# Kernel optimization log

Measured on AMD Instinct MI355X. Metric: run time of the kernel, lower is better.

Reference implementation:

```python
import jax, jax.numpy as jnp
import numpy as np

E = 1024        # embed_dim
NH = 16         # num_heads
HD = E // NH    # head_dim = 64
MLP = 4096
HID = int(2 * MLP / 3)  # 2730, TransNeXt ConvGLU hidden
NT = 1          # no_rope task tokens (skip rotary / skip dwconv)
B, S = 8, 1025
GRID = 32       # sqrt(S - NT)
EPS = 1e-6
SCALE = HD ** -0.5


def rmsnorm(x, g):
    return x * jax.lax.rsqrt(jnp.mean(x * x, axis=-1, keepdims=True) + EPS) * g


def apply_rope(t):
    # t: [B, NH, s, HD] -- rotate-half RoPE over image-token positions
    s = t.shape[2]
    pos = jnp.arange(s, dtype=jnp.float32)
    inv_freq = 1.0 / (10000.0 ** (jnp.arange(0, HD, 2, dtype=jnp.float32) / HD))
    freqs = pos[:, None] * inv_freq[None, :]          # [s, HD/2]
    cos = jnp.concatenate([jnp.cos(freqs)] * 2, -1)   # [s, HD]
    sin = jnp.concatenate([jnp.sin(freqs)] * 2, -1)
    t1, t2 = jnp.split(t, 2, axis=-1)
    rot = jnp.concatenate([-t2, t1], axis=-1)
    return t * cos + rot * sin


def rope_skip_task(t):
    # first NT tokens are task tokens -> identity; rest get rotary with positions 0..
    return jnp.concatenate([t[:, :, :NT], apply_rope(t[:, :, NT:])], axis=2)


def setup_inputs() -> dict:
    key = jax.random.key(0)
    ks = jax.random.split(key, 12)
    init = lambda k, shape, fan: (jax.random.normal(k, shape, jnp.float32) * (fan ** -0.5))
    return {
        "x": jax.random.normal(ks[0], (B, S, E), jnp.float32),
        "g1": jnp.ones((E,), jnp.float32),
        "w_qkv": init(ks[1], (E, 3 * E), E),
        "b_qkv": jnp.zeros((3 * E,), jnp.float32),
        "w_proj": init(ks[2], (E, E), E),
        "b_proj": jnp.zeros((E,), jnp.float32),
        "g2": jnp.ones((E,), jnp.float32),
        "fc1_w": init(ks[3], (E, 2 * HID), E),
        "fc1_b": jnp.zeros((2 * HID,), jnp.float32),
        "dw_w": init(ks[4], (3, 3, 1, HID), 9),  # HWIO depthwise 3x3
        "dw_b": jnp.zeros((HID,), jnp.float32),
        "fc2_w": init(ks[5], (HID, E), HID),
        "fc2_b": jnp.zeros((E,), jnp.float32),
    }


def reference(x, g1, w_qkv, b_qkv, w_proj, b_proj, g2, fc1_w, fc1_b, dw_w, dw_b, fc2_w, fc2_b):
    # ---- attention block ----
    residual = x
    xn = rmsnorm(x, g1)
    qkv = xn @ w_qkv + b_qkv                              # [B,S,3E]
    qkv = qkv.reshape(B, S, 3, NH, HD).transpose(2, 0, 3, 1, 4)
    q, k, v = qkv[0], qkv[1], qkv[2]                      # [B,NH,S,HD]
    q = rope_skip_task(q)
    k = rope_skip_task(k)
    attn = jnp.einsum("bhqd,bhkd->bhqk", q * SCALE, k)    # [B,NH,S,S]
    attn = jax.nn.softmax(attn, axis=-1)
    out = jnp.einsum("bhqk,bhkd->bhqd", attn, v)          # [B,NH,S,HD]
    out = out.transpose(0, 2, 1, 3).reshape(B, S, E)
    out = out @ w_proj + b_proj
    x = residual + out

    # ---- ConvGLU MLP block ----
    residual = x
    xn = rmsnorm(x, g2)
    h = xn @ fc1_w + fc1_b                                # [B,S,2*HID]
    xg, vg = jnp.split(h, 2, axis=-1)
    x_task, x_img = xg[:, :NT], xg[:, NT:]                # dwconv only on image tokens
    img = x_img.reshape(B, GRID, GRID, HID)
    img = jax.lax.conv_general_dilated(
        img, dw_w, window_strides=(1, 1), padding="SAME",
        feature_group_count=HID,
        dimension_numbers=("NHWC", "HWIO", "NHWC")) + dw_b
    x_img = img.reshape(B, GRID * GRID, HID)
    xc = jnp.concatenate([x_task, x_img], axis=1)
    h = jax.nn.gelu(xc, approximate=False) * vg           # GLU gate
    h = h @ fc2_w + fc2_b
    return residual + h
```

## Files before the change

kernel.cpp:

```cpp
#include <hip/hip_runtime.h>
#include <hip/hip_bf16.h>
#include <math.h>

#define E_DIM 1024
#define NHEAD 16
#define HID_DIM 2730
#define KP_FC2 2752
#define HB_LD 5504
#define XG_OFF 2752
#define FC1_N 5482
#define B_DIM 8
#define S_DIM 1025
#define EPS_V 1e-6f
#define SCALE_V 0.125f
#define MROWS (B_DIM * S_DIM)

typedef __attribute__((ext_vector_type(8))) short short8;
typedef __attribute__((ext_vector_type(4))) float f32x4;
typedef unsigned short us;

__device__ __forceinline__ float b2f(us u) {
    union { unsigned int i; float f; } x; x.i = ((unsigned int)u) << 16; return x.f;
}
__device__ __forceinline__ us f2b(float f) {
    __hip_bfloat16 h = __float2bfloat16(f);
    return *reinterpret_cast<us*>(&h);
}

__device__ __forceinline__ void stage16(const void* g, void* l) {
    __builtin_amdgcn_global_load_lds(
        (const __attribute__((address_space(1))) unsigned int*)g,
        (__attribute__((address_space(3))) unsigned int*)l,
        16, 0, 0);
}

__device__ __forceinline__ int sl(int row, int c8) {
    return (row * 8 + (c8 ^ (row & 7))) * 8;
}

#define MFMA16(a, b, c) __builtin_amdgcn_mfma_f32_16x16x32_bf16(a, b, c, 0, 0, 0)

__global__ __launch_bounds__(256) void rmsnorm_kernel(const float* __restrict__ x,
        const float* __restrict__ g, us* __restrict__ out) {
    int row = blockIdx.x;
    const float4* xr = (const float4*)(x + (size_t)row * E_DIM);
    float4 v = xr[threadIdx.x];
    float ss = v.x*v.x + v.y*v.y + v.z*v.z + v.w*v.w;
    #pragma unroll
    for (int off = 32; off > 0; off >>= 1) ss += __shfl_down(ss, off, 64);
    __shared__ float wsum[4];
    int lane = threadIdx.x & 63, w = threadIdx.x >> 6;
    if (lane == 0) wsum[w] = ss;
    __syncthreads();
    float tot = wsum[0] + wsum[1] + wsum[2] + wsum[3];
    float inv = rsqrtf(tot * (1.0f / E_DIM) + EPS_V);
    float4 gv = ((const float4*)g)[threadIdx.x];
    ushort4 o;
    o.x = f2b(v.x * inv * gv.x); o.y = f2b(v.y * inv * gv.y);
    o.z = f2b(v.z * inv * gv.z); o.w = f2b(v.w * inv * gv.w);
    ((ushort4*)(out + (size_t)row * E_DIM))[threadIdx.x] = o;
}

__global__ __launch_bounds__(256) void rmsnorm_add_kernel(float* __restrict__ x,
        const float* __restrict__ p, const float* __restrict__ g, us* __restrict__ out) {
    int row = blockIdx.x;
    float4* xr = (float4*)(x + (size_t)row * E_DIM);
    const float4* pr = (const float4*)(p + (size_t)row * E_DIM);
    float4 v = xr[threadIdx.x];
    float4 pv = pr[threadIdx.x];
    v.x += pv.x; v.y += pv.y; v.z += pv.z; v.w += pv.w;
    xr[threadIdx.x] = v;
    float ss = v.x*v.x + v.y*v.y + v.z*v.z + v.w*v.w;
    #pragma unroll
    for (int off = 32; off > 0; off >>= 1) ss += __shfl_down(ss, off, 64);
    __shared__ float wsum[4];
    int lane = threadIdx.x & 63, w = threadIdx.x >> 6;
    if (lane == 0) wsum[w] = ss;
    __syncthreads();
    float tot = wsum[0] + wsum[1] + wsum[2] + wsum[3];
    float inv = rsqrtf(tot * (1.0f / E_DIM) + EPS_V);
    float4 gv = ((const float4*)g)[threadIdx.x];
    ushort4 o;
    o.x = f2b(v.x * inv * gv.x); o.y = f2b(v.y * inv * gv.y);
    o.z = f2b(v.z * inv * gv.z); o.w = f2b(v.w * inv * gv.w);
    ((ushort4*)(out + (size_t)row * E_DIM))[threadIdx.x] = o;
}

__global__ __launch_bounds__(256) void addreduce_kernel(float* __restrict__ dst,
        const float* __restrict__ p, int n4) {
    int stride = gridDim.x * 256;
    for (int i = blockIdx.x * 256 + threadIdx.x; i < n4; i += stride) {
        float4 a = ((const float4*)p)[i];
        float4 d = ((float4*)dst)[i];
        d.x += a.x; d.y += a.y; d.z += a.z; d.w += a.w;
        ((float4*)dst)[i] = d;
    }
}

__global__ __launch_bounds__(256) void convt_kernel(const float* __restrict__ W,
        us* __restrict__ WT, int K, int N, int KPad, int swap_half, int xg_off, int Wld) {
    __shared__ float T[32][33];
    int n0 = blockIdx.x * 32, k0 = blockIdx.y * 32;
    int c = threadIdx.x & 31, r4 = (threadIdx.x >> 5) << 2;
    #pragma unroll
    for (int i = 0; i < 4; i++) {
        int k = k0 + r4 + i, n = n0 + c;
        float v = 0.0f;
        if (k < K && n < N) {
            int src = n;
            int ok = 1;
            if (swap_half) {
                if (n < swap_half) src = n + swap_half;
                else if (xg_off) { if (n >= xg_off) src = n - xg_off; else ok = 0; }
                else src = n - swap_half;
            }
            if (ok) v = W[(size_t)k * Wld + src];
        }
        T[c][r4 + i] = v;
    }
    __syncthreads();
    #pragma unroll
    for (int i = 0; i < 4; i++) {
        int n = n0 + r4 + i, k = k0 + c;
        if (n < N && k < KPad) WT[(size_t)n * KPad + k] = f2b(T[r4 + i][c]);
    }
}

__global__ __launch_bounds__(256) void bias_perm_kernel(const float* __restrict__ b,
        float* __restrict__ bp) {
    int r = blockIdx.x * 256 + threadIdx.x;
    if (r < FC1_N)
        bp[r] = (r < HID_DIM) ? b[r + HID_DIM] : ((r < XG_OFF) ? 0.0f : b[r - XG_OFF]);
}

template<int MODE>
__global__ __launch_bounds__(512, 2) void gemm256(const us* __restrict__ A, int lda,
        const us* __restrict__ Bt, int ldb, const float* __restrict__ bias,
        const float* __restrict__ Rres, void* __restrict__ Cv,
        int M, int N, int K, int ldc, int Ksplit, float* __restrict__ Pbuf) {
    __shared__ __align__(16) us lds[2][4][8192];
    us* const L = &lds[0][0][0];
    const int tid = threadIdx.x;
    const int lane = tid & 63;
    const int w = tid >> 6;
    const int wm = w >> 2, wn = w & 3;
    const int l15 = lane & 15, quad = lane >> 4;

    const int nwg = gridDim.x * gridDim.y;
    const int orig = blockIdx.y * gridDim.x + blockIdx.x;
    const int q8 = nwg >> 3, r8 = nwg & 7;
    const int xcd = orig & 7, oi = orig >> 3;
    const int wgid = (xcd < r8 ? xcd * (q8 + 1) : r8 * (q8 + 1) + (xcd - r8) * q8) + oi;
    const int m0 = (wgid / gridDim.x) * 256, n0 = (wgid % gridDim.x) * 256;

    const int kz = (MODE == 2) ? (int)blockIdx.z : 0;
    const int kofs = kz * Ksplit;
    const int Keff = (MODE == 2) ? (kz ? K - Ksplit : Ksplit) : K;

    const int r0 = tid >> 3;
    const int c80 = (tid & 7) ^ (r0 & 7);
    const us* const pA = A + (size_t)(m0 + r0) * lda + kofs + c80 * 8;
    const us* const pB = Bt + (size_t)(n0 + r0) * ldb + kofs + c80 * 8;
    const size_t a64 = (size_t)64 * lda, b64 = (size_t)64 * ldb;
    us* const dst = L + tid * 8;

#define STG_A(b, h, kt) do { \
    const us* s_ = pA + (size_t)(h) * 2 * a64 + (size_t)(kt) * 64; \
    stage16(s_,       dst + ((b) * 4 + (h)) * 8192); \
    stage16(s_ + a64, dst + ((b) * 4 + (h)) * 8192 + 4096); \
} while (0)
#define STG_B(b, h, kt) do { \
    const us* s_ = pB + (size_t)(h) * 2 * b64 + (size_t)(kt) * 64; \
    stage16(s_,       dst + ((b) * 4 + 2 + (h)) * 8192); \
    stage16(s_ + b64, dst + ((b) * 4 + 2 + (h)) * 8192 + 4096); \
} while (0)

    f32x4 acc[8][4];
    #pragma unroll
    for (int m = 0; m < 8; m++)
        #pragma unroll
        for (int n = 0; n < 4; n++) acc[m][n] = (f32x4){0.f, 0.f, 0.f, 0.f};

    const int nk = Keff >> 6;
    const int brow = (wn & 1) * 64;

    STG_A(0, 0, 0); STG_A(0, 1, 0);
    STG_B(0, 0, 0); STG_B(0, 1, 0);
    if (nk > 1) {
        STG_B(1, 0, 1); STG_B(1, 1, 1);
        STG_A(1, 0, 1); STG_A(1, 1, 1);
        asm volatile("s_waitcnt vmcnt(8)" ::: "memory");
    } else {
        asm volatile("s_waitcnt vmcnt(0)" ::: "memory");
    }
    __builtin_amdgcn_s_barrier();
    __builtin_amdgcn_sched_barrier(0);

    short8 bf01[2][2];
    {
        const us* bB0 = L + (2 + (wn >> 1)) * 8192;
        #pragma unroll
        for (int n = 0; n < 2; n++) {
            bf01[n][0] = *(const short8*)(bB0 + sl(brow + n * 16 + l15, quad));
            bf01[n][1] = *(const short8*)(bB0 + sl(brow + n * 16 + l15, 4 + quad));
        }
    }

    for (int t = 0; t < nk; t++) {
        const int c = t & 1, cn = c ^ 1;
        const us* aB = L + (c * 4 + wm) * 8192;
        const us* bB = L + (c * 4 + 2 + (wn >> 1)) * 8192;
        const us* bBn = L + (cn * 4 + 2 + (wn >> 1)) * 8192;
        short8 bf2[2][2];
        #pragma unroll
        for (int n = 0; n < 2; n++) {
            bf2[n][0] = *(const short8*)(bB + sl(brow + (n + 2) * 16 + l15, quad));
            bf2[n][1] = *(const short8*)(bB + sl(brow + (n + 2) * 16 + l15, 4 + quad));
        }
        #pragma unroll
        for (int p = 0; p < 4; p++) {
            const int mp = 2 * p;
            short8 a00 = *(const short8*)(aB + sl(mp * 16 + l15, quad));
            short8 a01 = *(const short8*)(aB + sl(mp * 16 + l15, 4 + quad));
            short8 a10 = *(const short8*)(aB + sl(mp * 16 + 16 + l15, quad));
            short8 a11 = *(const short8*)(aB + sl(mp * 16 + 16 + l15, 4 + quad));
            if (p == 1) { if (t + 2 < nk) STG_B(c, 0, t + 2); }
            else if (p == 2) { if (t + 2 < nk) STG_B(c, 1, t + 2); }
            else if (p == 3) {
                if (t + 2 < nk)      { asm volatile("s_waitcnt vmcnt(4)" ::: "memory"); }
                else if (t + 1 < nk) { asm volatile("s_waitcnt vmcnt(0)" ::: "memory"); }
            }
            __builtin_amdgcn_s_barrier();
            if (p == 3) __builtin_amdgcn_sched_barrier(0);
            __builtin_amdgcn_s_setprio(1);
            #pragma unroll
            for (int n = 0; n < 4; n++) {
                const short8 b0 = (n < 2) ? bf01[n][0] : bf2[n - 2][0];
                const short8 b1 = (n < 2) ? bf01[n][1] : bf2[n - 2][1];
                acc[mp][n]     = MFMA16(a00, b0, acc[mp][n]);
                acc[mp][n]     = MFMA16(a01, b1, acc[mp][n]);
                acc[mp + 1][n] = MFMA16(a10, b0, acc[mp + 1][n]);
                acc[mp + 1][n] = MFMA16(a11, b1, acc[mp + 1][n]);
            }
            __builtin_amdgcn_s_setprio(0);
            if (p == 3) {
                if (t + 2 < nk) { STG_A(c, 0, t + 2); STG_A(c, 1, t + 2); }
                if (t + 1 < nk) {
                    #pragma unroll
                    for (int n = 0; n < 2; n++) {
                        bf01[n][0] = *(const short8*)(bBn + sl(brow + n * 16 + l15, quad));
                        bf01[n][1] = *(const short8*)(bBn + sl(brow + n * 16 + l15, 4 + quad));
                    }
                }
            }
            __builtin_amdgcn_s_barrier();
            if (p == 3) __builtin_amdgcn_sched_barrier(0);
        }
    }

    #pragma unroll
    for (int m = 0; m < 8; m++) {
        int gm0 = m0 + wm * 128 + m * 16 + quad * 4;
        #pragma unroll
        for (int n = 0; n < 4; n++) {
            int gn = n0 + wn * 64 + n * 16 + l15;
            if (gn >= N) continue;
            float bs = (MODE == 2) ? (kz == 0 ? bias[gn] : 0.0f) : bias[gn];
            #pragma unroll
            for (int r = 0; r < 4; r++) {
                int gm = gm0 + r;
                if (gm >= M) continue;
                float v = acc[m][n][r] + bs;
                if (MODE == 0) {
                    ((us*)Cv)[(size_t)gm * ldc + gn] = f2b(v);
                } else if (MODE == 1) {
                    ((float*)Cv)[(size_t)gm * ldc + gn] = v + Rres[(size_t)gm * ldc + gn];
                } else {
                    if (kz == 0)
                        ((float*)Cv)[(size_t)gm * ldc + gn] = v + Rres[(size_t)gm * ldc + gn];
                    else
                        Pbuf[(size_t)gm * ldc + gn] = v;
                }
            }
        }
    }
#undef STG_A
#undef STG_B
}

__global__ __launch_bounds__(256) void rope_kernel(us* __restrict__ qkv) {
    int idx = blockIdx.x * 256 + threadIdx.x;
    int i = idx & 31;
    int h = (idx >> 5) & (NHEAD - 1);
    int rc = idx >> 9;
    int s = rc % S_DIM;
    us* q = qkv + (size_t)rc * 3072 + h * 64;
    us* k = q + 1024;
    if (s == 0) {
        q[i] = f2b(b2f(q[i]) * SCALE_V);
        q[i + 32] = f2b(b2f(q[i + 32]) * SCALE_V);
        return;
    }
    float pos = (float)(s - 1);
    float invf = expf((float)i * (-9.210340371976184f / 32.0f));
    float f = pos * invf;
    float c = cosf(f), sn = sinf(f);
    float q1 = b2f(q[i]), q2 = b2f(q[i + 32]);
    q[i]      = f2b((q1 * c - q2 * sn) * SCALE_V);
    q[i + 32] = f2b((q2 * c + q1 * sn) * SCALE_V);
    float k1 = b2f(k[i]), k2 = b2f(k[i + 32]);
    k[i]      = f2b(k1 * c - k2 * sn);
    k[i + 32] = f2b(k2 * c + k1 * sn);
}

__global__ __launch_bounds__(256) void vtrans_kernel(const us* __restrict__ qkv,
        us* __restrict__ Vt) {
    __shared__ us T[64][65];
    int st = blockIdx.x, h = blockIdx.y, bc = blockIdx.z;
    int tid = threadIdx.x;
    int r = tid & 63, cb = (tid >> 6) * 16;
    const us* src = qkv + (size_t)(bc * S_DIM + st * 64 + r) * 3072 + 2048 + h * 64 + cb;
    #pragma unroll
    for (int i = 0; i < 4; i++) {
        ushort4 v = *(const ushort4*)(src + i * 4);
        T[cb + i*4 + 0][r] = v.x; T[cb + i*4 + 1][r] = v.y;
        T[cb + i*4 + 2][r] = v.z; T[cb + i*4 + 3][r] = v.w;
    }
    __syncthreads();
    int d = tid >> 2, sc = (tid & 3) * 16;
    us* dstp = Vt + ((size_t)((bc * 16 + h) * 64 + d)) * 1088 + st * 64 + sc;
    #pragma unroll
    for (int g = 0; g < 4; g++) {
        ushort4 o;
        int i0 = sc + g * 4;
        o.x = (st*64 + i0 + 0 < S_DIM) ? T[d][i0 + 0] : 0;
        o.y = (st*64 + i0 + 1 < S_DIM) ? T[d][i0 + 1] : 0;
        o.z = (st*64 + i0 + 2 < S_DIM) ? T[d][i0 + 2] : 0;
        o.w = (st*64 + i0 + 3 < S_DIM) ? T[d][i0 + 3] : 0;
        *(ushort4*)(dstp + g * 4) = o;
    }
}

__global__ __launch_bounds__(256) void attn_kernel(const us* __restrict__ qkv,
        const us* __restrict__ Vt, us* __restrict__ attnb) {
    __shared__ __align__(16) us Kb[2][4096];
    __shared__ __align__(16) us Vb[2][4096];
    __shared__ __align__(16) us Ps[4096];
    int qt = blockIdx.x, h = blockIdx.y, bc = blockIdx.z;
    int tid = threadIdx.x;
    int lane = tid & 63, w = tid >> 6;
    int l15 = lane & 15, quad = lane >> 4;

    const us* qrow = qkv + (size_t)(bc * S_DIM + qt * 64 + 16 * w + l15) * 3072 + h * 64;
    short8 qa0 = *(const short8*)(qrow + quad * 8);
    short8 qa1 = *(const short8*)(qrow + 32 + quad * 8);

    const us* kg = qkv + (size_t)(bc * S_DIM) * 3072 + 1024 + h * 64;
    const us* vgp = Vt + (size_t)((bc * 16 + h) * 64) * 1088;

    int s0 = tid, s1 = 256 + tid;
    int row0 = s0 >> 3, c8_0 = (s0 & 7) ^ (row0 & 7);
    int row1 = s1 >> 3, c8_1 = (s1 & 7) ^ (row1 & 7);

    f32x4 acc_o[4];
    float mr[4], lr[4];
    #pragma unroll
    for (int r = 0; r < 4; r++) { mr[r] = -1e30f; lr[r] = 0.f; }
    #pragma unroll
    for (int j = 0; j < 4; j++) acc_o[j] = (f32x4){0.f, 0.f, 0.f, 0.f};

    stage16(kg + (size_t)row0 * 3072 + c8_0 * 8, Kb[0] + s0 * 8);
    stage16(vgp + (size_t)row0 * 1088 + c8_0 * 8, Vb[0] + s0 * 8);
    stage16(kg + (size_t)row1 * 3072 + c8_1 * 8, Kb[0] + s1 * 8);
    stage16(vgp + (size_t)row1 * 1088 + c8_1 * 8, Vb[0] + s1 * 8);
    __syncthreads();

    for (int kt = 0; kt < 17; kt++) {
        int cur = kt & 1, nxt = cur ^ 1;
        if (kt + 1 < 17) {
            stage16(kg + (size_t)((kt + 1) * 64 + row0) * 3072 + c8_0 * 8, Kb[nxt] + s0 * 8);
            stage16(vgp + (size_t)row0 * 1088 + (kt + 1) * 64 + c8_0 * 8, Vb[nxt] + s0 * 8);
            stage16(kg + (size_t)((kt + 1) * 64 + row1) * 3072 + c8_1 * 8, Kb[nxt] + s1 * 8);
            stage16(vgp + (size_t)row1 * 1088 + (kt + 1) * 64 + c8_1 * 8, Vb[nxt] + s1 * 8);
        }

        f32x4 accS[4];
        #pragma unroll
        for (int j = 0; j < 4; j++) accS[j] = (f32x4){0.f, 0.f, 0.f, 0.f};
        __builtin_amdgcn_s_setprio(1);
        #pragma unroll
        for (int j = 0; j < 4; j++) {
            short8 kb0 = *(const short8*)(Kb[cur] + sl(16 * j + l15, quad));
            short8 kb1 = *(const short8*)(Kb[cur] + sl(16 * j + l15, 4 + quad));
            accS[j] = MFMA16(qa0, kb0, accS[j]);
            accS[j] = MFMA16(qa1, kb1, accS[j]);
        }
        __builtin_amdgcn_s_setprio(0);

        #pragma unroll
        for (int j = 0; j < 4; j++) {
            if (kt * 64 + 16 * j + l15 >= S_DIM) {
                #pragma unroll
                for (int r = 0; r < 4; r++) accS[j][r] = -1e30f;
            }
        }

        float tm[4];
        #pragma unroll
        for (int r = 0; r < 4; r++) {
            float t = fmaxf(fmaxf(accS[0][r], accS[1][r]), fmaxf(accS[2][r], accS[3][r]));
            #pragma unroll
            for (int off = 1; off < 16; off <<= 1)
                t = fmaxf(t, __shfl_xor(t, off, 64));
            tm[r] = t;
        }
        int need = (tm[0] > mr[0] + 8.f) || (tm[1] > mr[1] + 8.f) ||
                   (tm[2] > mr[2] + 8.f) || (tm[3] > mr[3] + 8.f);
        if (__any(need)) {
            #pragma unroll
            for (int r = 0; r < 4; r++) {
                float mnew = fmaxf(mr[r], tm[r]);
                float al = __expf(mr[r] - mnew);
                mr[r] = mnew;
                lr[r] *= al;
                #pragma unroll
                for (int j = 0; j < 4; j++) acc_o[j][r] *= al;
            }
        }
        float pr[4][4];
        #pragma unroll
        for (int r = 0; r < 4; r++) {
            float rs = 0.f;
            #pragma unroll
            for (int j = 0; j < 4; j++) {
                float p = __expf(accS[j][r] - mr[r]);
                pr[j][r] = p;
                rs += p;
            }
            lr[r] += rs;
        }
        #pragma unroll
        for (int j = 0; j < 4; j++) {
            #pragma unroll
            for (int r = 0; r < 4; r++) {
                int prow = quad * 4 + r;
                int idx = sl(16 * w + prow, 2 * j + (l15 >> 3)) + (l15 & 7);
                Ps[idx] = f2b(pr[j][r]);
            }
        }
        short8 pa0 = *(const short8*)(Ps + sl(16 * w + l15, quad));
        short8 pa1 = *(const short8*)(Ps + sl(16 * w + l15, 4 + quad));
        __builtin_amdgcn_s_setprio(1);
        #pragma unroll
        for (int j = 0; j < 4; j++) {
            short8 vb0 = *(const short8*)(Vb[cur] + sl(16 * j + l15, quad));
            short8 vb1 = *(const short8*)(Vb[cur] + sl(16 * j + l15, 4 + quad));
            acc_o[j] = MFMA16(pa0, vb0, acc_o[j]);
            acc_o[j] = MFMA16(pa1, vb1, acc_o[j]);
        }
        __builtin_amdgcn_s_setprio(0);
        __syncthreads();
    }

    #pragma unroll
    for (int r = 0; r < 4; r++) {
        #pragma unroll
        for (int off = 1; off < 16; off <<= 1)
            lr[r] += __shfl_xor(lr[r], off, 64);
    }
    #pragma unroll
    for (int r = 0; r < 4; r++) {
        int s = qt * 64 + 16 * w + quad * 4 + r;
        if (s >= S_DIM) continue;
        float invl = 1.0f / lr[r];
        #pragma unroll
        for (int j = 0; j < 4; j++)
            attnb[(size_t)(bc * S_DIM + s) * E_DIM + h * 64 + 16 * j + l15] =
                f2b(acc_o[j][r] * invl);
    }
}

__global__ __launch_bounds__(256) void conv_gelu_kernel(us* __restrict__ hb,
        const float* __restrict__ dw_w, const float* __restrict__ dw_b) {
    int p = blockIdx.x % S_DIM;
    size_t row = blockIdx.x;
    size_t brow = row - p;
    int pp = p - 1;
    int gy = pp >> 5, gx = pp & 31;
    for (int g = threadIdx.x; g < 342; g += 256) {
        int c0 = g * 8;
        if (c0 + 8 <= HID_DIM) {
            float val[8];
            if (p == 0) {
                short8 xv = *(const short8*)(hb + row * HB_LD + XG_OFF + c0);
                #pragma unroll
                for (int e = 0; e < 8; e++) val[e] = b2f((us)xv[e]);
            } else {
                #pragma unroll
                for (int e = 0; e < 8; e++) val[e] = dw_b[c0 + e];
                #pragma unroll
                for (int dy = 0; dy < 3; dy++) {
                    int ny = gy + dy - 1;
                    if (ny < 0 || ny >= 32) continue;
                    #pragma unroll
                    for (int dx = 0; dx < 3; dx++) {
                        int nx = gx + dx - 1;
                        if (nx < 0 || nx >= 32) continue;
                        short8 xv = *(const short8*)(hb +
                                (brow + 1 + ny * 32 + nx) * HB_LD + XG_OFF + c0);
                        const float* wp = dw_w + (dy * 3 + dx) * HID_DIM + c0;
                        float2 w0 = *(const float2*)(wp);
                        float2 w1 = *(const float2*)(wp + 2);
                        float2 w2 = *(const float2*)(wp + 4);
                        float2 w3 = *(const float2*)(wp + 6);
                        val[0] = fmaf(b2f((us)xv[0]), w0.x, val[0]);
                        val[1] = fmaf(b2f((us)xv[1]), w0.y, val[1]);
                        val[2] = fmaf(b2f((us)xv[2]), w1.x, val[2]);
                        val[3] = fmaf(b2f((us)xv[3]), w1.y, val[3]);
                        val[4] = fmaf(b2f((us)xv[4]), w2.x, val[4]);
                        val[5] = fmaf(b2f((us)xv[5]), w2.y, val[5]);
                        val[6] = fmaf(b2f((us)xv[6]), w3.x, val[6]);
                        val[7] = fmaf(b2f((us)xv[7]), w3.y, val[7]);
                    }
                }
            }
            short8 gv = *(const short8*)(hb + row * HB_LD + c0);
            short8 o;
            #pragma unroll
            for (int e = 0; e < 8; e++) {
                float ge = 0.5f * val[e] * (1.0f + erff(val[e] * 0.70710678118654752f));
                o[e] = (short)f2b(ge * b2f((us)gv[e]));
            }
            *(short8*)(hb + row * HB_LD + c0) = o;
        } else {
            for (int c = c0; c < HID_DIM; c++) {
                float val;
                if (p == 0) {
                    val = b2f(hb[row * HB_LD + XG_OFF + c]);
                } else {
                    float a = dw_b[c];
                    #pragma unroll
                    for (int dy = 0; dy < 3; dy++) {
                        int ny = gy + dy - 1;
                        if (ny < 0 || ny >= 32) continue;
                        #pragma unroll
                        for (int dx = 0; dx < 3; dx++) {
                            int nx = gx + dx - 1;
                            if (nx < 0 || nx >= 32) continue;
                            a = fmaf(b2f(hb[(brow + 1 + ny * 32 + nx) * HB_LD + XG_OFF + c]),
                                     dw_w[(dy * 3 + dx) * HID_DIM + c], a);
                        }
                    }
                    val = a;
                }
                float ge = 0.5f * val * (1.0f + erff(val * 0.70710678118654752f));
                hb[row * HB_LD + c] = f2b(ge * b2f(hb[row * HB_LD + c]));
            }
        }
    }
}

static size_t ws_need(int cb) {
    size_t R = (size_t)cb * 1025, Rp = ((R + 127) / 128) * 128;
    size_t end1 = Rp*1024*2 + Rp*3072*2 + (size_t)cb*16*64*1088*2
                + 8320ull*1024*2 + 3072ull*1024*2 + 1024ull*1024*2;
    size_t end2 = Rp*1024*2 + Rp*HB_LD*2 + 5504ull*1024*2 + 1024ull*KP_FC2*2 + 5504*4;
    return end1 > end2 ? end1 : end2;
}

extern "C" void kernel_launch(void* const* d_in, const int* in_sizes, int n_in,
                              void* d_out, int out_size, void* d_ws, size_t ws_size,
                              hipStream_t stream) {
    const float* x      = (const float*)d_in[0];
    const float* g1     = (const float*)d_in[1];
    const float* w_qkv  = (const float*)d_in[2];
    const float* b_qkv  = (const float*)d_in[3];
    const float* w_proj = (const float*)d_in[4];
    const float* b_proj = (const float*)d_in[5];
    const float* g2     = (const float*)d_in[6];
    const float* fc1_w  = (const float*)d_in[7];
    const float* fc1_b  = (const float*)d_in[8];
    const float* dw_w   = (const float*)d_in[9];
    const float* dw_b   = (const float*)d_in[10];
    const float* fc2_w  = (const float*)d_in[11];
    const float* fc2_b  = (const float*)d_in[12];
    float* out = (float*)d_out;
    char* base = (char*)d_ws;

    int CB = 2;
    if (ws_size >= ws_need(8)) CB = 8;
    else if (ws_size >= ws_need(4)) CB = 4;
    int NC = B_DIM / CB;
    size_t R = (size_t)CB * 1025, Rp = ((R + 127) / 128) * 128;
    int gy256 = (int)((R + 255) / 256);
    int gyM = (MROWS + 255) / 256;

    size_t pOff = ((ws_need(CB) + 255) / 256) * 256;
    size_t pBytes = (size_t)MROWS * E_DIM * 4;
    int use_split = (ws_size >= pOff + pBytes);
    float* P1 = (float*)(base + pOff);

    us* xn    = (us*)base;
    size_t o  = Rp * 1024 * 2;
    us* qkv   = (us*)(base + o);
    us* hbuf  = (us*)(base + o);
    size_t o2 = o + Rp * 3072 * 2;
    us* Vt    = (us*)(base + o2);
    size_t o3 = o2 + (size_t)CB * 16 * 64 * 1088 * 2;
    us* attnb = (us*)(base + o3);
    size_t o4 = o3 + 8320ull * 1024 * 2;
    us* qkvT  = (us*)(base + o4);
    size_t o5 = o4 + 3072ull * 1024 * 2;
    us* projT = (us*)(base + o5);
    size_t p2 = o + Rp * HB_LD * 2;
    us* fc1T  = (us*)(base + p2);
    size_t p3 = p2 + 5504ull * 1024 * 2;
    us* fc2T  = (us*)(base + p3);
    float* fc1bp = (float*)(base + p3 + 1024ull * KP_FC2 * 2);

    convt_kernel<<<dim3(96, 32), 256, 0, stream>>>(w_qkv, qkvT, 1024, 3072, 1024, 0, 0, 3072);
    convt_kernel<<<dim3(32, 32), 256, 0, stream>>>(w_proj, projT, 1024, 1024, 1024, 0, 0, 1024);
    for (int c = 0; c < NC; c++) {
        size_t roff = (size_t)c * R;
        rmsnorm_kernel<<<(int)R, 256, 0, stream>>>(x + roff * E_DIM, g1, xn);
        gemm256<0><<<dim3(12, gy256), 512, 0, stream>>>(xn, 1024, qkvT, 1024,
                b_qkv, nullptr, qkv, (int)R, 3072, 1024, 3072, 0, nullptr);
        rope_kernel<<<(int)(2 * R), 256, 0, stream>>>(qkv);
        vtrans_kernel<<<dim3(17, 16, CB), 256, 0, stream>>>(qkv, Vt);
        attn_kernel<<<dim3(17, 16, CB), 256, 0, stream>>>(qkv, Vt, attnb + roff * E_DIM);
    }
    if (use_split) {
        gemm256<2><<<dim3(4, gyM, 2), 512, 0, stream>>>(attnb, 1024, projT, 1024,
                b_proj, x, out, MROWS, 1024, 1024, 1024, 512, P1);
    } else {
        gemm256<1><<<dim3(4, gyM), 512, 0, stream>>>(attnb, 1024, projT, 1024,
                b_proj, x, out, MROWS, 1024, 1024, 1024, 0, nullptr);
    }

    convt_kernel<<<dim3(172, 32), 256, 0, stream>>>(fc1_w, fc1T, 1024, FC1_N, 1024,
            HID_DIM, XG_OFF, 5460);
    convt_kernel<<<dim3(32, 86), 256, 0, stream>>>(fc2_w, fc2T, HID_DIM, 1024, KP_FC2,
            0, 0, 1024);
    bias_perm_kernel<<<22, 256, 0, stream>>>(fc1_b, fc1bp);
    for (int c = 0; c < NC; c++) {
        size_t roff = (size_t)c * R;
        float* outc = out + roff * E_DIM;
        if (use_split) {
            rmsnorm_add_kernel<<<(int)R, 256, 0, stream>>>(outc, P1 + roff * E_DIM, g2, xn);
        } else {
            rmsnorm_kernel<<<(int)R, 256, 0, stream>>>(outc, g2, xn);
        }
        gemm256<0><<<dim3(22, gy256), 512, 0, stream>>>(xn, 1024, fc1T, 1024,
                fc1bp, nullptr, hbuf, (int)R, FC1_N, 1024, HB_LD, 0, nullptr);
        conv_gelu_kernel<<<(int)R, 256, 0, stream>>>(hbuf, dw_w, dw_b);
        if (use_split) {
            gemm256<2><<<dim3(4, gy256, 2), 512, 0, stream>>>(hbuf, HB_LD, fc2T, KP_FC2,
                    fc2_b, outc, outc, (int)R, 1024, KP_FC2, 1024, 1408, P1 + roff * E_DIM);
            addreduce_kernel<<<2048, 256, 0, stream>>>(outc, P1 + roff * E_DIM,
                    (int)(R * 256));
        } else {
            gemm256<1><<<dim3(4, gy256), 512, 0, stream>>>(hbuf, HB_LD, fc2T, KP_FC2,
                    fc2_b, outc, outc, (int)R, 1024, KP_FC2, 1024, 0, nullptr);
        }
    }
}
```

Baseline: 783.1 us.

## Add software-pipelined GEMM variant with XCD-aware tile remap for fc1

Adds a new 256x256 bf16 MFMA GEMM kernel used only for the fc1 projection. It double-buffers LDS stages two K-tiles ahead, interleaves global loads with MFMA phases under explicit waitcnt, barriers and priority hints, and remaps workgroup IDs so neighbouring tiles land on the same XCD for L2 reuse. The aim is to hide global-load latency and improve cache locality in the largest GEMM. The price is a large, hand-scheduled kernel whose behaviour depends on compiler scheduling and occupancy (launch bounds of 2 blocks with 128KB LDS).

```diff
diff --git a/kernel.cpp b/kernel.cpp
--- a/kernel.cpp
+++ b/kernel.cpp
@@ -286,6 +286,127 @@
     }
 #undef STG_A
 #undef STG_B
+}
+
+__global__ __launch_bounds__(512, 2) void gemm256v2(const us* __restrict__ A, int lda,
+        const us* __restrict__ Bt, int ldb, const float* __restrict__ bias,
+        void* __restrict__ Cv, int M, int N, int K, int ldc) {
+    __shared__ __align__(16) us lds[2][32768];
+    us* const L = &lds[0][0];
+    const int tid = threadIdx.x;
+    const int lane = tid & 63;
+    const int w = tid >> 6;
+    const int wm = w >> 2, wn = w & 3;
+    const int l15 = lane & 15, quad = lane >> 4;
+
+    const int nwg = gridDim.x * gridDim.y;
+    const int orig = blockIdx.y * gridDim.x + blockIdx.x;
+    const int q8 = nwg >> 3, r8 = nwg & 7;
+    const int xcd = orig & 7, oi = orig >> 3;
+    const int wgid = (xcd < r8 ? xcd * (q8 + 1) : r8 * (q8 + 1) + (xcd - r8) * q8) + oi;
+    const int m0 = (wgid / gridDim.x) * 256, n0 = (wgid % gridDim.x) * 256;
+
+    const int a_lr = (tid >> 3) & 31;
+    const int a_c8 = (tid & 7) ^ (a_lr & 7);
+    const us* const pA2 = A + (size_t)(m0 + ((tid >> 8) << 7) + a_lr) * lda + a_c8 * 8;
+    const int r0 = tid >> 3;
+    const int c80 = (tid & 7) ^ (r0 & 7);
+    const us* const pB = Bt + (size_t)(n0 + r0) * ldb + c80 * 8;
+    const size_t a32 = (size_t)32 * lda, b64 = (size_t)64 * ldb;
+
+#define STG_A2(b, u, kt) \
+    stage16(pA2 + (size_t)(u) * a32 + (size_t)(kt) * 64, \
+            L + (b) * 32768 + (u) * 4096 + tid * 8)
+#define STG_B2(b, h, kt) do { \
+    const us* s_ = pB + (size_t)(h) * 2 * b64 + (size_t)(kt) * 64; \
+    stage16(s_,       L + (b) * 32768 + 16384 + (h) * 8192 + tid * 8); \
+    stage16(s_ + b64, L + (b) * 32768 + 16384 + (h) * 8192 + 4096 + tid * 8); \
+} while (0)
+
+    f32x4 acc[8][4];
+    #pragma unroll
+    for (int m = 0; m < 8; m++)
+        #pragma unroll
+        for (int n = 0; n < 4; n++) acc[m][n] = (f32x4){0.f, 0.f, 0.f, 0.f};
+
+    const int nk = K >> 6;
+    const int brow = (wn & 1) * 64;
+
+    STG_B2(0, 0, 0); STG_B2(0, 1, 0);
+    STG_A2(0, 0, 0); STG_A2(0, 1, 0); STG_A2(0, 2, 0); STG_A2(0, 3, 0);
+    if (nk > 1) {
+        STG_B2(1, 0, 1); STG_B2(1, 1, 1);
+        STG_A2(1, 0, 1); STG_A2(1, 1, 1); STG_A2(1, 2, 1); STG_A2(1, 3, 1);
+        asm volatile("s_waitcnt vmcnt(8)" ::: "memory");
+    } else {
+        asm volatile("s_waitcnt vmcnt(0)" ::: "memory");
+    }
+    __builtin_amdgcn_s_barrier();
+    __builtin_amdgcn_sched_barrier(0);
+
+    for (int t = 0; t < nk; t++) {
+        const int c = t & 1;
+        const us* aBt = L + c * 32768;
+        const us* bBt = L + c * 32768 + 16384 + (wn >> 1) * 8192;
+        short8 bf[4][2];
+        #pragma unroll
+        for (int p = 0; p < 4; p++) {
+            if (p == 0) {
+                #pragma unroll
+                for (int n = 0; n < 4; n++) {
+                    bf[n][0] = *(const short8*)(bBt + sl(brow + n * 16 + l15, quad));
+                    bf[n][1] = *(const short8*)(bBt + sl(brow + n * 16 + l15, 4 + quad));
+                }
+            }
+            const us* aU = aBt + p * 4096 + wm * 2048;
+            short8 a00 = *(const short8*)(aU + sl(l15, quad));
+            short8 a01 = *(const short8*)(aU + sl(l15, 4 + quad));
+            short8 a10 = *(const short8*)(aU + sl(16 + l15, quad));
+            short8 a11 = *(const short8*)(aU + sl(16 + l15, 4 + quad));
+            if (t + 2 < nk) {
+                if (p == 0)      { STG_B2(c, 0, t + 2); STG_A2(c, 0, t + 2); }
+                else if (p == 1) { STG_B2(c, 1, t + 2); STG_A2(c, 1, t + 2); }
+                else if (p == 2) { STG_A2(c, 2, t + 2); }
+                else             { STG_A2(c, 3, t + 2); }
+            }
+            if (p == 3) {
+                if (t + 2 < nk)      { asm volatile("s_waitcnt vmcnt(8)" ::: "memory"); }
+                else if (t + 1 < nk) { asm volatile("s_waitcnt vmcnt(0)" ::: "memory"); }
+            }
+            __builtin_amdgcn_s_barrier();
+            if (p == 3) __builtin_amdgcn_sched_barrier(0);
+            __builtin_amdgcn_s_setprio(1);
+            #pragma unroll
+            for (int n = 0; n < 4; n++) {
+                acc[2 * p][n]     = MFMA16(a00, bf[n][0], acc[2 * p][n]);
+                acc[2 * p][n]     = MFMA16(a01, bf[n][1], acc[2 * p][n]);
+                acc[2 * p + 1][n] = MFMA16(a10, bf[n][0], acc[2 * p + 1][n]);
+                acc[2 * p + 1][n] = MFMA16(a11, bf[n][1], acc[2 * p + 1][n]);
+            }
+            __builtin_amdgcn_s_setprio(0);
+            __builtin_amdgcn_s_barrier();
+            if (p == 3) __builtin_amdgcn_sched_barrier(0);
+        }
+    }
+
+    #pragma unroll
+    for (int m = 0; m < 8; m++) {
+        int gm0 = m0 + wm * 128 + m * 16 + quad * 4;
+        #pragma unroll
+        for (int n = 0; n < 4; n++) {
+            int gn = n0 + wn * 64 + n * 16 + l15;
+            if (gn >= N) continue;
+            float bs = bias[gn];
+            #pragma unroll
+            for (int r = 0; r < 4; r++) {
+                int gm = gm0 + r;
+                if (gm >= M) continue;
+                ((us*)Cv)[(size_t)gm * ldc + gn] = f2b(acc[m][n][r] + bs);
+            }
+        }
+    }
+#undef STG_A2
+#undef STG_B2
 }
 
 __global__ __launch_bounds__(256) void rope_kernel(us* __restrict__ qkv) {
@@ -650,8 +771,8 @@
         } else {
             rmsnorm_kernel<<<(int)R, 256, 0, stream>>>(outc, g2, xn);
         }
-        gemm256<0><<<dim3(22, gy256), 512, 0, stream>>>(xn, 1024, fc1T, 1024,
-                fc1bp, nullptr, hbuf, (int)R, FC1_N, 1024, HB_LD, 0, nullptr);
+        gemm256v2<<<dim3(22, gy256), 512, 0, stream>>>(xn, 1024, fc1T, 1024,
+                fc1bp, hbuf, (int)R, FC1_N, 1024, HB_LD);
         conv_gelu_kernel<<<(int)R, 256, 0, stream>>>(hbuf, dw_w, dw_b);
         if (use_split) {
             gemm256<2><<<dim3(4, gy256, 2), 512, 0, stream>>>(hbuf, HB_LD, fc2T, KP_FC2,
```

After: 793.5 us. No clear change (+1.3%).
